# Kernel optimization log

Measured on AMD Instinct MI355X. Metric: run time of the kernel, lower is better.

## Reference

```python
import jax, jax.numpy as jnp
import numpy as np

B, S, D, H = 2, 2048, 2048, 8  # n_seq must equal hidden_dim (attn_net consumes the key axis)
DK = D // H
SCALING = DK ** -0.5
NEG = -1e9  # stand-in for -inf so fp16/bf16 also work


def setup_inputs() -> dict:
    key = jax.random.key(0)
    ks = jax.random.split(key, 12)
    w = lambda k, shp: (jax.random.normal(k, shp, dtype=jnp.float32) * 0.02)
    return {
        "x": jax.random.normal(ks[0], (B, S, D), dtype=jnp.float32),
        "x_mask": jax.random.randint(ks[1], (1, S), 0, 2).astype(jnp.int32),  # 1 = masked
        "Wq": w(ks[2], (D, D)), "bq": jnp.zeros((D,), jnp.float32),
        "Wk": w(ks[3], (D, D)), "bk": jnp.zeros((D,), jnp.float32),
        "Wv": w(ks[4], (D, D)), "bv": jnp.zeros((D,), jnp.float32),
        "Wa": w(ks[5], (D,)),   "ba": jnp.zeros((1,), jnp.float32),
        "Wp": w(ks[6], (D, D)), "bp": jnp.zeros((D,), jnp.float32),
    }


def reference(x, x_mask, Wq, bq, Wk, bk, Wv, bv, Wa, ba, Wp, bp):
    b, s, d = x.shape
    heads = lambda t: t.reshape(b, s, H, DK).transpose(0, 2, 1, 3)  # [B,H,S,DK]
    q = heads(x @ Wq.T + bq)
    k = heads(x @ Wk.T + bk)
    v = heads(x @ Wv.T + bv)
    # custom additive attention: QK^T -> leaky_relu -> linear score -> scale
    e = jax.nn.leaky_relu(jnp.einsum('bhid,bhjd->bhij', q, k), 0.1)   # [B,H,S,S]
    score = SCALING * (jnp.einsum('bhij,j->bhi', e, Wa) + ba[0])      # [B,H,S] one score per token
    # mask-fill (masked_fill semantics: True -> -inf) then softmax over tokens
    score = jnp.where(x_mask[:, None, :] != 0, NEG, score)
    attn = jax.nn.softmax(score, axis=-1)                             # [B,H,S]
    out = jnp.einsum('bhs,bhsd->bhd', attn, v).reshape(b, d)          # pooled [B,D]
    return jnp.tanh(out @ Wp.T + bp)                                  # [B,D]
```

## Files before the change

kernel.cpp:

```cpp
#include <hip/hip_runtime.h>
#include <hip/hip_bf16.h>
#include <stdint.h>

#define B_ 2
#define S_ 2048
#define D_ 2048
#define H_ 8
#define DK_ 256
#define SCALE_ 0.0625f
#define NEG_ -1e9f

typedef __hip_bfloat16 bf16;
typedef __attribute__((ext_vector_type(4))) float f32x4;
typedef __attribute__((ext_vector_type(8))) short bf16x8;
typedef unsigned int u32;

__device__ inline void gload_lds16(const void* g, void* l) {
  __builtin_amdgcn_global_load_lds(
      (const __attribute__((address_space(1))) u32*)g,
      (__attribute__((address_space(3))) u32*)l, 16, 0, 0);
}

__global__ void cvt_kernel(const float* __restrict__ in, bf16* __restrict__ out, int n4) {
  int i = blockIdx.x * 256 + threadIdx.x;
  if (i >= n4) return;
  float4 v = ((const float4*)in)[i];
  ushort4 o;
  o.x = __builtin_bit_cast(unsigned short, __float2bfloat16(v.x));
  o.y = __builtin_bit_cast(unsigned short, __float2bfloat16(v.y));
  o.z = __builtin_bit_cast(unsigned short, __float2bfloat16(v.z));
  o.w = __builtin_bit_cast(unsigned short, __float2bfloat16(v.w));
  ((ushort4*)out)[i] = o;
}

__global__ __launch_bounds__(256, 2) void gemm_qk(
    const bf16* __restrict__ A,
    const bf16* __restrict__ W0, const float* __restrict__ b0, bf16* __restrict__ C0,
    const bf16* __restrict__ W1, const float* __restrict__ b1, bf16* __restrict__ C1) {
  const int Kd = D_;
  const bf16* Bm = blockIdx.z ? W1 : W0;
  const float* bias = blockIdx.z ? b1 : b0;
  bf16* C = blockIdx.z ? C1 : C0;

  __shared__ bf16 As[128 * 64];
  __shared__ bf16 Bs[128 * 64];
  const int tid = threadIdx.x;
  const int lane = tid & 63;
  const int w = tid >> 6;
  const int wr = w >> 1, wc = w & 1;
  const int bm = blockIdx.y, bn = blockIdx.x;

  f32x4 acc[4][4] = {};
  const int l8r = lane >> 3;
  const int l8c = (lane & 7) * 8;

  for (int kt = 0; kt < Kd; kt += 64) {
#pragma unroll
    for (int cc = 0; cc < 4; ++cc) {
      int chunk = w * 4 + cc;
      int rowa = bm * 128 + chunk * 8 + l8r;
      gload_lds16(A + (size_t)rowa * Kd + kt + l8c, (char*)As + chunk * 1024);
      int rowb = bn * 128 + chunk * 8 + l8r;
      gload_lds16(Bm + (size_t)rowb * Kd + kt + l8c, (char*)Bs + chunk * 1024);
    }
    __syncthreads();
#pragma unroll
    for (int kk = 0; kk < 2; ++kk) {
      const int kloc = kk * 32 + (lane >> 4) * 8;
      bf16x8 af[4], bfr[4];
#pragma unroll
      for (int mi = 0; mi < 4; ++mi) {
        int row = wr * 64 + mi * 16 + (lane & 15);
        af[mi] = *(const bf16x8*)&As[row * 64 + kloc];
      }
#pragma unroll
      for (int ni = 0; ni < 4; ++ni) {
        int row = wc * 64 + ni * 16 + (lane & 15);
        bfr[ni] = *(const bf16x8*)&Bs[row * 64 + kloc];
      }
#pragma unroll
      for (int mi = 0; mi < 4; ++mi)
#pragma unroll
        for (int ni = 0; ni < 4; ++ni)
          acc[mi][ni] = __builtin_amdgcn_mfma_f32_16x16x32_bf16(af[mi], bfr[ni], acc[mi][ni], 0, 0, 0);
    }
    __syncthreads();
  }
#pragma unroll
  for (int ni = 0; ni < 4; ++ni) {
    int col = bn * 128 + wc * 64 + ni * 16 + (lane & 15);
    int h = col >> 8, dk = col & 255;
    float bb = bias[col];
#pragma unroll
    for (int mi = 0; mi < 4; ++mi) {
      int rbase = bm * 128 + wr * 64 + mi * 16 + (lane >> 4) * 4;
#pragma unroll
      for (int r = 0; r < 4; ++r) {
        int row = rbase + r;
        int b = row >> 11, s = row & 2047;
        C[(((size_t)b * H_ + h) * S_ + s) * DK_ + dk] = __float2bfloat16(acc[mi][ni][r] + bb);
      }
    }
  }
}

__global__ __launch_bounds__(256, 1) void score_kernel(
    const bf16* __restrict__ Qh, const bf16* __restrict__ Kh,
    const float* __restrict__ Wa, float* __restrict__ score) {
  __shared__ bf16 Ks[2][128 * 256];
  __shared__ float sred[2][128];
  const int tid = threadIdx.x, lane = tid & 63, w = tid >> 6;
  const int wr = w >> 1, wc = w & 1;
  const int bh = blockIdx.x;
  const int it = blockIdx.y;

  const bf16* Qbase = Qh + (size_t)bh * S_ * DK_;
  const bf16* Kbase = Kh + (size_t)bh * S_ * DK_;

  bf16x8 qf[4][8];
#pragma unroll
  for (int mi = 0; mi < 4; ++mi) {
    int row = it * 128 + wr * 64 + mi * 16 + (lane & 15);
    const bf16* qp = Qbase + (size_t)row * DK_ + ((lane >> 4) * 8);
#pragma unroll
    for (int kc = 0; kc < 8; ++kc) qf[mi][kc] = *(const bf16x8*)(qp + kc * 32);
  }

  const int stg_r_sub = lane >> 5;
  const int stg_b = (lane & 31) * 16;
  auto STAGE = [&](int buf, int jt) {
    const char* src = (const char*)(Kbase + (size_t)jt * 128 * DK_);
#pragma unroll
    for (int cc = 0; cc < 16; ++cc) {
      int chunk = w * 16 + cc;
      int r = chunk * 2 + stg_r_sub;
      int gb = stg_b ^ ((r & 7) << 4);
      gload_lds16(src + (size_t)r * 512 + gb, (char*)&Ks[buf][0] + chunk * 1024);
    }
  };

  STAGE(0, 0);
  __syncthreads();

  float psum[4][4] = {};
  for (int jt = 0; jt < 16; ++jt) {
    const int cur = jt & 1;
    if (jt + 1 < 16) STAGE(cur ^ 1, jt + 1);
    const char* Kc = (const char*)&Ks[cur][0];
#pragma unroll
    for (int nj = 0; nj < 4; ++nj) {
      int jloc = wc * 64 + nj * 16 + (lane & 15);
      bf16x8 bfr[8];
#pragma unroll
      for (int kc = 0; kc < 8; ++kc) {
        int kbyte = (kc * 32 + ((lane >> 4) * 8)) * 2;
        bfr[kc] = *(const bf16x8*)(Kc + jloc * 512 + (kbyte ^ ((jloc & 7) << 4)));
      }
      f32x4 cf[4] = {};
#pragma unroll
      for (int kc = 0; kc < 8; ++kc)
#pragma unroll
        for (int mi = 0; mi < 4; ++mi)
          cf[mi] = __builtin_amdgcn_mfma_f32_16x16x32_bf16(qf[mi][kc], bfr[kc], cf[mi], 0, 0, 0);
      float wa = Wa[jt * 128 + jloc];
#pragma unroll
      for (int mi = 0; mi < 4; ++mi)
#pragma unroll
        for (int r = 0; r < 4; ++r) {
          float v = cf[mi][r];
          v = (v > 0.f) ? v : 0.1f * v;
          psum[mi][r] += v * wa;
        }
    }
    __syncthreads();
  }
#pragma unroll
  for (int mi = 0; mi < 4; ++mi)
#pragma unroll
    for (int r = 0; r < 4; ++r) {
      float v = psum[mi][r];
      v += __shfl_xor(v, 1); v += __shfl_xor(v, 2);
      v += __shfl_xor(v, 4); v += __shfl_xor(v, 8);
      if ((lane & 15) == 0) {
        int lrow = wr * 64 + mi * 16 + ((lane >> 4) * 4) + r;
        sred[wc][lrow] = v;
      }
    }
  __syncthreads();
  if (tid < 128)
    score[(size_t)bh * S_ + it * 128 + tid] = sred[0][tid] + sred[1][tid];
}

__global__ __launch_bounds__(256) void softmax_kernel(
    const float* __restrict__ score, const int* __restrict__ xmask,
    const float* __restrict__ ba, float* __restrict__ attn) {
  const int bh = blockIdx.x, tid = threadIdx.x;
  const int lane = tid & 63, w = tid >> 6;
  __shared__ float redm[4], reds[4];
  const float ba0 = ba[0];
  float loc[8];
  float mx = -3.4e38f;
#pragma unroll
  for (int t = 0; t < 8; ++t) {
    int i = t * 256 + tid;
    float s = SCALE_ * (score[(size_t)bh * S_ + i] + ba0);
    if (xmask[i] != 0) s = NEG_;
    loc[t] = s;
    mx = fmaxf(mx, s);
  }
  for (int m = 1; m < 64; m <<= 1) mx = fmaxf(mx, __shfl_xor(mx, m));
  if (lane == 0) redm[w] = mx;
  __syncthreads();
  mx = fmaxf(fmaxf(redm[0], redm[1]), fmaxf(redm[2], redm[3]));
  float sum = 0.f;
#pragma unroll
  for (int t = 0; t < 8; ++t) {
    loc[t] = expf(loc[t] - mx);
    sum += loc[t];
  }
  for (int m = 1; m < 64; m <<= 1) sum += __shfl_xor(sum, m);
  if (lane == 0) reds[w] = sum;
  __syncthreads();
  sum = reds[0] + reds[1] + reds[2] + reds[3];
  const float inv = 1.f / sum;
#pragma unroll
  for (int t = 0; t < 8; ++t) attn[(size_t)bh * S_ + t * 256 + tid] = loc[t] * inv;
}

__global__ __launch_bounds__(256) void xbar_kernel(
    const float* __restrict__ x, const float* __restrict__ attn, float* __restrict__ xbar) {
  const int cblk = blockIdx.x, sblk = blockIdx.y, b = blockIdx.z;
  const int tid = threadIdx.x;
  const int c = cblk * 1024 + tid * 4;
  __shared__ float at_s[8][32];
  for (int i = tid; i < 8 * 32; i += 256) {
    int h = i >> 5, s = i & 31;
    at_s[h][s] = attn[((size_t)b * H_ + h) * S_ + sblk * 32 + s];
  }
  __syncthreads();
  float acc[8][4] = {};
  const float* xp = x + ((size_t)b * S_ + sblk * 32) * D_ + c;
#pragma unroll 8
  for (int s = 0; s < 32; ++s) {
    float4 xv = *(const float4*)(xp + (size_t)s * D_);
#pragma unroll
    for (int h = 0; h < 8; ++h) {
      float a = at_s[h][s];
      acc[h][0] += a * xv.x; acc[h][1] += a * xv.y;
      acc[h][2] += a * xv.z; acc[h][3] += a * xv.w;
    }
  }
#pragma unroll
  for (int h = 0; h < 8; ++h)
#pragma unroll
    for (int e = 0; e < 4; ++e)
      atomicAdd(&xbar[((size_t)b * H_ + h) * D_ + c + e], acc[h][e]);
}

__global__ __launch_bounds__(256) void pooled_kernel(
    const float* __restrict__ xbar, const float* __restrict__ Wv,
    const float* __restrict__ bv, float* __restrict__ pooled) {
  const int lane = threadIdx.x & 63;
  const int dv = blockIdx.x * 4 + (threadIdx.x >> 6);
  const int h = dv >> 8;
  const float* wrow = Wv + (size_t)dv * D_;
  const float* x0 = xbar + (size_t)h * D_;
  const float* x1 = xbar + (size_t)(H_ + h) * D_;
  float a0 = 0.f, a1 = 0.f;
  for (int c = lane; c < D_; c += 64) {
    float wv = wrow[c];
    a0 += wv * x0[c];
    a1 += wv * x1[c];
  }
  for (int m = 1; m < 64; m <<= 1) { a0 += __shfl_xor(a0, m); a1 += __shfl_xor(a1, m); }
  if (lane == 0) {
    float bb = bv[dv];
    pooled[dv] = a0 + bb;
    pooled[D_ + dv] = a1 + bb;
  }
}

__global__ __launch_bounds__(256) void final_kernel(
    const float* __restrict__ pooled, const float* __restrict__ Wp,
    const float* __restrict__ bp, float* __restrict__ out) {
  const int lane = threadIdx.x & 63;
  const int n = blockIdx.x * 4 + (threadIdx.x >> 6);
  const float* wrow = Wp + (size_t)n * D_;
  float a0 = 0.f, a1 = 0.f;
  for (int c = lane; c < D_; c += 64) {
    float wv = wrow[c];
    a0 += wv * pooled[c];
    a1 += wv * pooled[D_ + c];
  }
  for (int m = 1; m < 64; m <<= 1) { a0 += __shfl_xor(a0, m); a1 += __shfl_xor(a1, m); }
  if (lane == 0) {
    float bb = bp[n];
    out[n] = tanhf(a0 + bb);
    out[D_ + n] = tanhf(a1 + bb);
  }
}

extern "C" void kernel_launch(void* const* d_in, const int* in_sizes, int n_in,
                              void* d_out, int out_size, void* d_ws, size_t ws_size,
                              hipStream_t stream) {
  const float* x = (const float*)d_in[0];
  const int* xmask = (const int*)d_in[1];
  const float* Wq = (const float*)d_in[2];
  const float* bq = (const float*)d_in[3];
  const float* Wk = (const float*)d_in[4];
  const float* bk = (const float*)d_in[5];
  const float* Wv = (const float*)d_in[6];
  const float* bv = (const float*)d_in[7];
  const float* Wa = (const float*)d_in[8];
  const float* ba = (const float*)d_in[9];
  const float* Wp = (const float*)d_in[10];
  const float* bp = (const float*)d_in[11];
  float* out = (float*)d_out;

  char* ws = (char*)d_ws;
  bf16* Xb = (bf16*)ws;    ws += (size_t)B_ * S_ * D_ * 2;
  bf16* Wqb = (bf16*)ws;   ws += (size_t)D_ * D_ * 2;
  bf16* Wkb = (bf16*)ws;   ws += (size_t)D_ * D_ * 2;
  bf16* Qb = (bf16*)ws;    ws += (size_t)B_ * S_ * D_ * 2;
  bf16* Kbf = (bf16*)ws;   ws += (size_t)B_ * S_ * D_ * 2;
  float* score = (float*)ws;  ws += (size_t)B_ * H_ * S_ * 4;
  float* attn = (float*)ws;   ws += (size_t)B_ * H_ * S_ * 4;
  float* xbar = (float*)ws;   ws += (size_t)B_ * H_ * D_ * 4;
  float* pooled = (float*)ws; ws += (size_t)B_ * D_ * 4;

  const int nX4 = B_ * S_ * D_ / 4, nW4 = D_ * D_ / 4;
  cvt_kernel<<<nX4 / 256, 256, 0, stream>>>(x, Xb, nX4);
  cvt_kernel<<<nW4 / 256, 256, 0, stream>>>(Wq, Wqb, nW4);
  cvt_kernel<<<nW4 / 256, 256, 0, stream>>>(Wk, Wkb, nW4);

  gemm_qk<<<dim3(D_ / 128, B_ * S_ / 128, 2), 256, 0, stream>>>(
      Xb, Wqb, bq, Qb, Wkb, bk, Kbf);

  score_kernel<<<dim3(B_ * H_, S_ / 128), 256, 0, stream>>>(Qb, Kbf, Wa, score);

  softmax_kernel<<<B_ * H_, 256, 0, stream>>>(score, xmask, ba, attn);

  hipMemsetAsync(xbar, 0, (size_t)B_ * H_ * D_ * 4, stream);
  xbar_kernel<<<dim3(2, 64, B_), 256, 0, stream>>>(x, attn, xbar);

  pooled_kernel<<<D_ / 4, 256, 0, stream>>>(xbar, Wv, bv, pooled);
  final_kernel<<<D_ / 4, 256, 0, stream>>>(pooled, Wp, bp, out);
}
```

Before: 373.7 us.

## Merge bf16 conversions, retile score kernel without LDS, replace xbar atomics

The three fp32-to-bf16 conversion launches become one kernel that routes each index to the right tensor. The score kernel drops its double-buffered LDS staging of K, loads K fragments straight from global memory, and uses 64-row Q tiles with two blocks per CU, which doubles the grid and halves register pressure. The xbar atomics and memset are replaced by per-block partial sums written into the reused Wq bf16 buffer plus a separate deterministic reduce kernel. The risk is that global K loads without LDS reuse raise memory traffic in the dominant score kernel.

```diff
diff --git a/kernel.cpp b/kernel.cpp
--- a/kernel.cpp
+++ b/kernel.cpp
@@ -21,16 +21,22 @@
       (__attribute__((address_space(3))) u32*)l, 16, 0, 0);
 }
 
-__global__ void cvt_kernel(const float* __restrict__ in, bf16* __restrict__ out, int n4) {
+__global__ void cvt_all_kernel(const float* __restrict__ x, bf16* __restrict__ xo,
+                               const float* __restrict__ wq, bf16* __restrict__ wqo,
+                               const float* __restrict__ wk, bf16* __restrict__ wko,
+                               int nX4, int nW4) {
   int i = blockIdx.x * 256 + threadIdx.x;
-  if (i >= n4) return;
-  float4 v = ((const float4*)in)[i];
+  const float* in; bf16* out; int idx;
+  if (i < nX4) { in = x; out = xo; idx = i; }
+  else if (i < nX4 + nW4) { in = wq; out = wqo; idx = i - nX4; }
+  else { in = wk; out = wko; idx = i - nX4 - nW4; }
+  float4 v = ((const float4*)in)[idx];
   ushort4 o;
   o.x = __builtin_bit_cast(unsigned short, __float2bfloat16(v.x));
   o.y = __builtin_bit_cast(unsigned short, __float2bfloat16(v.y));
   o.z = __builtin_bit_cast(unsigned short, __float2bfloat16(v.z));
   o.w = __builtin_bit_cast(unsigned short, __float2bfloat16(v.w));
-  ((ushort4*)out)[i] = o;
+  ((ushort4*)out)[idx] = o;
 }
 
 __global__ __launch_bounds__(256, 2) void gemm_qk(
@@ -104,11 +110,10 @@
   }
 }
 
-__global__ __launch_bounds__(256, 1) void score_kernel(
+__global__ __launch_bounds__(256, 2) void score_kernel(
     const bf16* __restrict__ Qh, const bf16* __restrict__ Kh,
     const float* __restrict__ Wa, float* __restrict__ score) {
-  __shared__ bf16 Ks[2][128 * 256];
-  __shared__ float sred[2][128];
+  __shared__ float sred[2][64];
   const int tid = threadIdx.x, lane = tid & 63, w = tid >> 6;
   const int wr = w >> 1, wc = w & 1;
   const int bh = blockIdx.x;
@@ -117,54 +122,35 @@
   const bf16* Qbase = Qh + (size_t)bh * S_ * DK_;
   const bf16* Kbase = Kh + (size_t)bh * S_ * DK_;
 
-  bf16x8 qf[4][8];
-#pragma unroll
-  for (int mi = 0; mi < 4; ++mi) {
-    int row = it * 128 + wr * 64 + mi * 16 + (lane & 15);
+  bf16x8 qf[2][8];
+#pragma unroll
+  for (int mi = 0; mi < 2; ++mi) {
+    int row = it * 64 + wr * 32 + mi * 16 + (lane & 15);
     const bf16* qp = Qbase + (size_t)row * DK_ + ((lane >> 4) * 8);
 #pragma unroll
     for (int kc = 0; kc < 8; ++kc) qf[mi][kc] = *(const bf16x8*)(qp + kc * 32);
   }
 
-  const int stg_r_sub = lane >> 5;
-  const int stg_b = (lane & 31) * 16;
-  auto STAGE = [&](int buf, int jt) {
-    const char* src = (const char*)(Kbase + (size_t)jt * 128 * DK_);
-#pragma unroll
-    for (int cc = 0; cc < 16; ++cc) {
-      int chunk = w * 16 + cc;
-      int r = chunk * 2 + stg_r_sub;
-      int gb = stg_b ^ ((r & 7) << 4);
-      gload_lds16(src + (size_t)r * 512 + gb, (char*)&Ks[buf][0] + chunk * 1024);
-    }
-  };
-
-  STAGE(0, 0);
-  __syncthreads();
-
-  float psum[4][4] = {};
+  float psum[2][4] = {};
+  const int koff = (lane >> 4) * 8;
+
   for (int jt = 0; jt < 16; ++jt) {
-    const int cur = jt & 1;
-    if (jt + 1 < 16) STAGE(cur ^ 1, jt + 1);
-    const char* Kc = (const char*)&Ks[cur][0];
-#pragma unroll
+#pragma unroll 2
     for (int nj = 0; nj < 4; ++nj) {
-      int jloc = wc * 64 + nj * 16 + (lane & 15);
+      int jrow = jt * 128 + wc * 64 + nj * 16 + (lane & 15);
+      const bf16* kp = Kbase + (size_t)jrow * DK_ + koff;
       bf16x8 bfr[8];
 #pragma unroll
-      for (int kc = 0; kc < 8; ++kc) {
-        int kbyte = (kc * 32 + ((lane >> 4) * 8)) * 2;
-        bfr[kc] = *(const bf16x8*)(Kc + jloc * 512 + (kbyte ^ ((jloc & 7) << 4)));
-      }
-      f32x4 cf[4] = {};
+      for (int kc = 0; kc < 8; ++kc) bfr[kc] = *(const bf16x8*)(kp + kc * 32);
+      f32x4 cf[2] = {};
 #pragma unroll
       for (int kc = 0; kc < 8; ++kc)
 #pragma unroll
-        for (int mi = 0; mi < 4; ++mi)
+        for (int mi = 0; mi < 2; ++mi)
           cf[mi] = __builtin_amdgcn_mfma_f32_16x16x32_bf16(qf[mi][kc], bfr[kc], cf[mi], 0, 0, 0);
-      float wa = Wa[jt * 128 + jloc];
-#pragma unroll
-      for (int mi = 0; mi < 4; ++mi)
+      float wa = Wa[jrow];
+#pragma unroll
+      for (int mi = 0; mi < 2; ++mi)
 #pragma unroll
         for (int r = 0; r < 4; ++r) {
           float v = cf[mi][r];
@@ -172,23 +158,22 @@
           psum[mi][r] += v * wa;
         }
     }
-    __syncthreads();
-  }
-#pragma unroll
-  for (int mi = 0; mi < 4; ++mi)
+  }
+#pragma unroll
+  for (int mi = 0; mi < 2; ++mi)
 #pragma unroll
     for (int r = 0; r < 4; ++r) {
       float v = psum[mi][r];
       v += __shfl_xor(v, 1); v += __shfl_xor(v, 2);
       v += __shfl_xor(v, 4); v += __shfl_xor(v, 8);
       if ((lane & 15) == 0) {
-        int lrow = wr * 64 + mi * 16 + ((lane >> 4) * 4) + r;
+        int lrow = wr * 32 + mi * 16 + ((lane >> 4) * 4) + r;
         sred[wc][lrow] = v;
       }
     }
   __syncthreads();
-  if (tid < 128)
-    score[(size_t)bh * S_ + it * 128 + tid] = sred[0][tid] + sred[1][tid];
+  if (tid < 64)
+    score[(size_t)bh * S_ + it * 64 + tid] = sred[0][tid] + sred[1][tid];
 }
 
 __global__ __launch_bounds__(256) void softmax_kernel(
@@ -227,8 +212,8 @@
   for (int t = 0; t < 8; ++t) attn[(size_t)bh * S_ + t * 256 + tid] = loc[t] * inv;
 }
 
-__global__ __launch_bounds__(256) void xbar_kernel(
-    const float* __restrict__ x, const float* __restrict__ attn, float* __restrict__ xbar) {
+__global__ __launch_bounds__(256) void xbar_part_kernel(
+    const float* __restrict__ x, const float* __restrict__ attn, float* __restrict__ part) {
   const int cblk = blockIdx.x, sblk = blockIdx.y, b = blockIdx.z;
   const int tid = threadIdx.x;
   const int c = cblk * 1024 + tid * 4;
@@ -250,11 +235,20 @@
       acc[h][2] += a * xv.z; acc[h][3] += a * xv.w;
     }
   }
+  float* pp = part + (((size_t)sblk * B_ + b) * H_) * D_ + c;
 #pragma unroll
   for (int h = 0; h < 8; ++h)
-#pragma unroll
-    for (int e = 0; e < 4; ++e)
-      atomicAdd(&xbar[((size_t)b * H_ + h) * D_ + c + e], acc[h][e]);
+    *(float4*)(pp + (size_t)h * D_) = *(const float4*)&acc[h][0];
+}
+
+__global__ __launch_bounds__(256) void xbar_reduce_kernel(
+    const float* __restrict__ part, float* __restrict__ xbar) {
+  const int idx = blockIdx.x * 256 + threadIdx.x;
+  float s = 0.f;
+#pragma unroll 8
+  for (int sb = 0; sb < 64; ++sb)
+    s += part[(size_t)sb * (B_ * H_ * D_) + idx];
+  xbar[idx] = s;
 }
 
 __global__ __launch_bounds__(256) void pooled_kernel(
@@ -327,21 +321,21 @@
   float* attn = (float*)ws;   ws += (size_t)B_ * H_ * S_ * 4;
   float* xbar = (float*)ws;   ws += (size_t)B_ * H_ * D_ * 4;
   float* pooled = (float*)ws; ws += (size_t)B_ * D_ * 4;
+  float* part = (float*)Wqb;
 
   const int nX4 = B_ * S_ * D_ / 4, nW4 = D_ * D_ / 4;
-  cvt_kernel<<<nX4 / 256, 256, 0, stream>>>(x, Xb, nX4);
-  cvt_kernel<<<nW4 / 256, 256, 0, stream>>>(Wq, Wqb, nW4);
-  cvt_kernel<<<nW4 / 256, 256, 0, stream>>>(Wk, Wkb, nW4);
+  cvt_all_kernel<<<(nX4 + 2 * nW4) / 256, 256, 0, stream>>>(
+      x, Xb, Wq, Wqb, Wk, Wkb, nX4, nW4);
 
   gemm_qk<<<dim3(D_ / 128, B_ * S_ / 128, 2), 256, 0, stream>>>(
       Xb, Wqb, bq, Qb, Wkb, bk, Kbf);
 
-  score_kernel<<<dim3(B_ * H_, S_ / 128), 256, 0, stream>>>(Qb, Kbf, Wa, score);
+  score_kernel<<<dim3(B_ * H_, S_ / 64), 256, 0, stream>>>(Qb, Kbf, Wa, score);
 
   softmax_kernel<<<B_ * H_, 256, 0, stream>>>(score, xmask, ba, attn);
 
-  hipMemsetAsync(xbar, 0, (size_t)B_ * H_ * D_ * 4, stream);
-  xbar_kernel<<<dim3(2, 64, B_), 256, 0, stream>>>(x, attn, xbar);
+  xbar_part_kernel<<<dim3(2, 64, B_), 256, 0, stream>>>(x, attn, part);
+  xbar_reduce_kernel<<<B_ * H_ * D_ / 256, 256, 0, stream>>>(part, xbar);
 
   pooled_kernel<<<D_ / 4, 256, 0, stream>>>(xbar, Wv, bv, pooled);
   final_kernel<<<D_ / 4, 256, 0, stream>>>(pooled, Wp, bp, out);
```

New measurement: 398.1 us. +6.5%, slower.
